# Optimization experiments

Measured on AMD Instinct MI355X. Metric: run time of the kernel, lower is better.

The kernel has to match this reference:

```python
import jax, jax.numpy as jnp
import numpy as np

B, L, C, H, W = 2, 48, 8, 48, 48


def setup_inputs() -> dict:
    key = jax.random.key(0)
    k1, k2 = jax.random.split(key)
    flows = jax.random.normal(k1, (B, L, 2, H, W), dtype=jnp.float32) * 0.05
    images = jax.random.normal(k2, (B, L, C, H, W), dtype=jnp.float32)
    return {"flows": flows, "images": images}


def _base_grid(Hh, Ww, dtype):
    step_y, step_x = 2.0 / Hh, 2.0 / Ww
    gy = jnp.linspace(-1.0 + 0.5 * step_y, 1.0 - 0.5 * step_y, Hh, dtype=dtype)
    gx = jnp.linspace(-1.0 + 0.5 * step_x, 1.0 - 0.5 * step_x, Ww, dtype=dtype)
    GX, GY = jnp.meshgrid(gx, gy, indexing="xy")  # each (H, W)
    return jnp.stack([GX, GY], axis=-1)  # (H, W, 2), channel 0 = x


def _sample_bilinear(img, ix, iy):
    # img: (C, H, W); ix, iy: (H, W) pixel coords (align_corners=False),
    # padding_mode='zeros'. 4-tap bilinear with zero outside [0, size-1].
    Hh, Ww = img.shape[1], img.shape[2]
    x0 = jnp.floor(ix)
    y0 = jnp.floor(iy)
    wx1 = ix - x0
    wy1 = iy - y0

    def tap(xf, yf, w):
        valid = (xf >= 0) & (xf <= Ww - 1) & (yf >= 0) & (yf <= Hh - 1)
        xc = jnp.clip(xf.astype(jnp.int32), 0, Ww - 1)
        yc = jnp.clip(yf.astype(jnp.int32), 0, Hh - 1)
        return img[:, yc, xc] * (w * valid)[None]

    return (tap(x0, y0, (1 - wx1) * (1 - wy1))
            + tap(x0 + 1, y0, wx1 * (1 - wy1))
            + tap(x0, y0 + 1, (1 - wx1) * wy1)
            + tap(x0 + 1, y0 + 1, wx1 * wy1))


def reference(flows, images):
    Bb, Ll, Cc, Hh, Ww = images.shape
    dtype = flows.dtype
    cum = jnp.cumsum(flows.astype(jnp.float32), axis=1).astype(dtype)  # (B,L,2,H,W)
    k_idx, t_idx = jnp.triu_indices(Ll)  # P pairs, k <= t

    base = _base_grid(Hh, Ww, dtype)  # (H,W,2)
    rel = cum[:, t_idx] - cum[:, k_idx]              # (B,P,2,H,W)
    grid = base + jnp.moveaxis(rel, 2, -1)           # (B,P,H,W,2)
    gx = jnp.remainder(grid[..., 0] + 1.0, 2.0) - 1.0  # wrap x only
    gy = grid[..., 1]
    # align_corners=False unnormalize: ((g+1)*size - 1) / 2
    ix = ((gx + 1.0) * Ww - 1.0) * 0.5
    iy = ((gy + 1.0) * Hh - 1.0) * 0.5

    src = images[:, k_idx]                           # (B,P,C,H,W)
    warped = jax.vmap(jax.vmap(_sample_bilinear))(src, ix, iy)  # (B,P,C,H,W)
    # scatter-accumulate each warped pair into its target frame t
    out = jax.vmap(lambda w: jax.ops.segment_sum(w, t_idx, num_segments=Ll))(warped)
    return out  # (B,L,C,H,W)
```

## Files before the change

kernel.cpp:

```cpp
#include <hip/hip_runtime.h>
#include <hip/hip_fp16.h>

constexpr int B = 2, L = 48, C = 8, H = 48, W = 48;
constexpr int HW = H * W;

constexpr int TPB    = 256;
constexpr int CHUNKS = HW / TPB;
constexpr int NOCT   = 6;

constexpr int OUT_ELEMS = B * L * C * HW;

constexpr int NCUM        = B * 2 * HW;
constexpr int CUM_BLOCKS  = NCUM / 256;
constexpr int NCONV       = B * L * HW;
constexpr int CONV_BLOCKS = (NCONV + 255) / 256;

__global__ void prep_kernel(const float* __restrict__ flows,
                            const float* __restrict__ images,
                            float* __restrict__ cum2,
                            __half* __restrict__ imgH) {
    if (blockIdx.x < CUM_BLOCKS) {
        int tid  = blockIdx.x * 256 + threadIdx.x;
        int pix  = tid % HW;
        int comp = (tid / HW) & 1;
        int b    = tid / (2 * HW);
        const float* src = flows + (size_t)b * L * 2 * HW + (size_t)comp * HW + pix;
        float*       dst = cum2  + ((size_t)b * L * HW + pix) * 2 + comp;
        float acc = 0.0f;
#pragma unroll
        for (int l = 0; l < L; ++l) {
            acc += src[(size_t)l * 2 * HW];
            dst[(size_t)l * HW * 2] = acc;
        }
    } else {
        int tid = (blockIdx.x - CUM_BLOCKS) * 256 + threadIdx.x;
        if (tid >= NCONV) return;
        int pix = tid % HW;
        int bl  = tid / HW;
        const float* src = images + (size_t)bl * C * HW + pix;
        __half h[C];
#pragma unroll
        for (int c = 0; c < C; ++c) h[c] = __float2half(src[(size_t)c * HW]);
        float4* dst = reinterpret_cast<float4*>(imgH + ((size_t)bl * HW + pix) * C);
        *dst = *reinterpret_cast<float4*>(h);
    }
}

struct SampleGeom {
    float w00, w10, w01, w11;
    int x0, y0;
};

__device__ __forceinline__ SampleGeom sample_geom(float base_gx_p1, float base_gy,
                                                  float relx, float rely) {
    float v = base_gx_p1 + relx;
    v = (v >= 2.0f) ? v - 2.0f : v;
    v = (v >= 2.0f) ? v - 2.0f : v;
    v = (v >= 2.0f) ? v - 2.0f : v;
    v = (v <  0.0f) ? v + 2.0f : v;
    v = (v <  0.0f) ? v + 2.0f : v;
    v = (v <  0.0f) ? v + 2.0f : v;

    float ix = (v * (float)W - 1.0f) * 0.5f;
    float gy = base_gy + rely;
    float iy = ((gy + 1.0f) * (float)H - 1.0f) * 0.5f;

    float x0f = floorf(ix), y0f = floorf(iy);
    float wx1 = ix - x0f,   wy1 = iy - y0f;
    float wx0 = 1.0f - wx1, wy0 = 1.0f - wy1;

    float vx0 = (x0f >= 0.0f  && x0f <= (float)(W - 1)) ? 1.0f : 0.0f;
    float vx1 = (x0f >= -1.0f && x0f <= (float)(W - 2)) ? 1.0f : 0.0f;
    float vy0 = (y0f >= 0.0f  && y0f <= (float)(H - 1)) ? 1.0f : 0.0f;
    float vy1 = (y0f >= -1.0f && y0f <= (float)(H - 2)) ? 1.0f : 0.0f;

    SampleGeom g;
    g.w00 = wx0 * wy0 * vx0 * vy0;
    g.w10 = wx1 * wy0 * vx1 * vy0;
    g.w01 = wx0 * wy1 * vx0 * vy1;
    g.w11 = wx1 * wy1 * vx1 * vy1;
    g.x0  = (int)x0f;
    g.y0  = (int)y0f;
    return g;
}

#if defined(__has_builtin)
#if __has_builtin(__builtin_amdgcn_global_load_lds)
#define HAVE_GLD_LDS 1
#endif
#endif

__device__ __forceinline__ void stage_frame(const __half* __restrict__ gsrc,
                                            __half* lds_base, int tid) {
#ifdef HAVE_GLD_LDS
#pragma unroll
    for (int i = 0; i < 9; ++i) {
        const int r = i * 256 + tid;
        __builtin_amdgcn_global_load_lds(
            (const __attribute__((address_space(1))) void*)(gsrc + (size_t)r * C),
            (__attribute__((address_space(3))) void*)(lds_base + (size_t)r * C),
            16, 0, 0);
    }
#else
#pragma unroll
    for (int i = 0; i < 9; ++i) {
        const int r = i * 256 + tid;
        float4 v = *reinterpret_cast<const float4*>(gsrc + (size_t)r * C);
        *reinterpret_cast<float4*>(lds_base + (size_t)r * C) = v;
    }
#endif
}

__device__ __forceinline__ void gather_mix(const __half* fb, const SampleGeom& g,
                                           float acc[C]) {
    int x0 = min(max(g.x0,     0), W - 1);
    int x1 = min(max(g.x0 + 1, 0), W - 1);
    int y0 = min(max(g.y0,     0), H - 1);
    int y1 = min(max(g.y0 + 1, 0), H - 1);
    float4 r00 = *reinterpret_cast<const float4*>(fb + (y0 * W + x0) * C);
    float4 r10 = *reinterpret_cast<const float4*>(fb + (y0 * W + x1) * C);
    float4 r01 = *reinterpret_cast<const float4*>(fb + (y1 * W + x0) * C);
    float4 r11 = *reinterpret_cast<const float4*>(fb + (y1 * W + x1) * C);
    auto mix = [&](const float4& raw, float wgt) {
        const __half2* hc = reinterpret_cast<const __half2*>(&raw);
#pragma unroll
        for (int c = 0; c < 4; ++c) {
            float2 f = __half22float2(hc[c]);
            acc[2 * c]     += wgt * f.x;
            acc[2 * c + 1] += wgt * f.y;
        }
    };
    mix(r00, g.w00); mix(r10, g.w10); mix(r01, g.w01); mix(r11, g.w11);
}

template <int P>
__global__ __launch_bounds__(256) void scan_oct_kernel(const float* __restrict__ cum2,
                                                       const __half* __restrict__ imgH,
                                                       float* __restrict__ out,
                                                       float* __restrict__ part) {
    const int tid  = threadIdx.x;
    const int pix0 = blockIdx.x * TPB;
    const int pix  = pix0 + tid;
    const int g    = blockIdx.y;
    const int par  = blockIdx.z % P;
    const int b    = blockIdx.z / P;

    int tj[8];
#pragma unroll
    for (int j = 0; j < 4; ++j) {
        tj[2 * j]     = 12 * j + g;
        tj[2 * j + 1] = 12 * j + 11 - g;
    }
    const int kmax = 47 - g;

    const int w = pix % W;
    const int h = pix / W;
    const float base_gx_p1 = (2 * w + 1) * (1.0f / W);
    const float base_gy    = (2 * h + 1) * (1.0f / H) - 1.0f;

    const float* cb = cum2 + ((size_t)b * L * HW + pix) * 2;
    float ctx[8], cty[8];
#pragma unroll
    for (int j = 0; j < 8; ++j) {
        float2 c = *reinterpret_cast<const float2*>(cb + (size_t)tj[j] * HW * 2);
        ctx[j] = c.x; cty[j] = c.y;
    }

    float acc[8][C];
#pragma unroll
    for (int j = 0; j < 8; ++j)
#pragma unroll
        for (int c = 0; c < C; ++c) acc[j][c] = 0.0f;

    __shared__ __align__(16) unsigned char smem[2 * HW * C * 2];
    __half* fr0 = reinterpret_cast<__half*>(smem);
    __half* fr1 = reinterpret_cast<__half*>(smem + HW * C * 2);

    const __half* gb = imgH + (size_t)b * L * HW * C;

    stage_frame(gb + (size_t)par * HW * C, fr0, tid);
    float2 ck = *reinterpret_cast<const float2*>(cb + (size_t)par * HW * 2);
    __syncthreads();

    int cur = 0;
    for (int k = par; k <= kmax; k += P) {
        __half* nb = cur ? fr0 : fr1;
        const __half* fb = cur ? fr1 : fr0;
        if (k + P <= kmax)
            stage_frame(gb + (size_t)(k + P) * HW * C, nb, tid);
        float2 ckn = ck;
        if (k + P <= kmax)
            ckn = *reinterpret_cast<const float2*>(cb + (size_t)(k + P) * HW * 2);

#pragma unroll
        for (int j = 0; j < 8; ++j) {
            if (tj[j] >= k) {
                SampleGeom gm = sample_geom(base_gx_p1, base_gy,
                                            ctx[j] - ck.x, cty[j] - ck.y);
                gather_mix(fb, gm, acc[j]);
            }
        }

        ck = ckn;
        __syncthreads();
        cur ^= 1;
    }

    float* accT = reinterpret_cast<float*>(smem);
#pragma unroll
    for (int j = 0; j < 8; ++j)
#pragma unroll
        for (int c = 0; c < C; ++c)
            accT[(j * 8 + c) * TPB + tid] = acc[j][c];
    __syncthreads();

    float* dst = (par == 0) ? out : (part + (size_t)(par - 1) * OUT_ELEMS);
    const int lane = tid & 63;
    const int wv   = tid >> 6;
#pragma unroll
    for (int r = 0; r < 16; ++r) {
        int pl = wv + 4 * r;
        int j  = pl >> 3, c = pl & 7;
        float4 v = *reinterpret_cast<float4*>(&accT[pl * TPB + lane * 4]);
        *reinterpret_cast<float4*>(dst + ((size_t)(b * L + tj[j]) * C + c) * HW
                                   + pix0 + lane * 4) = v;
    }
}

template <int P>
__global__ void reduce_kernel(float* __restrict__ out, const float* __restrict__ part) {
    int i = blockIdx.x * blockDim.x + threadIdx.x;
    constexpr int N4 = OUT_ELEMS / 4;
    if (i < N4) {
        float4 a = reinterpret_cast<float4*>(out)[i];
#pragma unroll
        for (int p = 0; p < P - 1; ++p) {
            float4 q = reinterpret_cast<const float4*>(part + (size_t)p * OUT_ELEMS)[i];
            a.x += q.x; a.y += q.y; a.z += q.z; a.w += q.w;
        }
        reinterpret_cast<float4*>(out)[i] = a;
    }
}

extern "C" void kernel_launch(void* const* d_in, const int* in_sizes, int n_in,
                              void* d_out, int out_size, void* d_ws, size_t ws_size,
                              hipStream_t stream) {
    const float* flows  = (const float*)d_in[0];
    const float* images = (const float*)d_in[1];
    float* out = (float*)d_out;

    const size_t cum_elems  = (size_t)B * L * 2 * HW;
    const size_t imgH_elems = (size_t)B * L * HW * C;

    float*  cum2 = (float*)d_ws;
    __half* imgH = (__half*)(cum2 + cum_elems);
    float*  part = (float*)(imgH + imgH_elems);

    const size_t base_bytes = cum_elems * 4 + imgH_elems * 2;
    const size_t out_bytes  = (size_t)OUT_ELEMS * 4;

    prep_kernel<<<CUM_BLOCKS + CONV_BLOCKS, 256, 0, stream>>>(flows, images, cum2, imgH);

    constexpr int N4 = OUT_ELEMS / 4;
    const int rblocks = (N4 + 255) / 256;

    if (ws_size >= base_bytes + 3 * out_bytes) {
        dim3 grid(CHUNKS, NOCT, 2 * 4);
        scan_oct_kernel<4><<<grid, 256, 0, stream>>>(cum2, imgH, out, part);
        reduce_kernel<4><<<rblocks, 256, 0, stream>>>(out, part);
    } else if (ws_size >= base_bytes + 2 * out_bytes) {
        dim3 grid(CHUNKS, NOCT, 2 * 3);
        scan_oct_kernel<3><<<grid, 256, 0, stream>>>(cum2, imgH, out, part);
        reduce_kernel<3><<<rblocks, 256, 0, stream>>>(out, part);
    } else {
        dim3 grid(CHUNKS, NOCT, 2 * 2);
        scan_oct_kernel<2><<<grid, 256, 0, stream>>>(cum2, imgH, out, part);
        reduce_kernel<2><<<rblocks, 256, 0, stream>>>(out, part);
    }
}
```

Measured before the change: 51.84 us.

## Generalize scan over target groups, store partial sums in half, use 8-way k split

```diff
diff --git a/kernel.cpp b/kernel.cpp
--- a/kernel.cpp
+++ b/kernel.cpp
@@ -6,7 +6,6 @@
 
 constexpr int TPB    = 256;
 constexpr int CHUNKS = HW / TPB;
-constexpr int NOCT   = 6;
 
 constexpr int OUT_ELEMS = B * L * C * HW;
 
@@ -133,11 +132,12 @@
     mix(r00, g.w00); mix(r10, g.w10); mix(r01, g.w01); mix(r11, g.w11);
 }
 
-template <int P>
-__global__ __launch_bounds__(256) void scan_oct_kernel(const float* __restrict__ cum2,
-                                                       const __half* __restrict__ imgH,
-                                                       float* __restrict__ out,
-                                                       float* __restrict__ part) {
+template <int TT, int P>
+__global__ __launch_bounds__(256) void scan_kernel(const float* __restrict__ cum2,
+                                                   const __half* __restrict__ imgH,
+                                                   float* __restrict__ out,
+                                                   __half* __restrict__ part) {
+    constexpr int S = 96 / TT;
     const int tid  = threadIdx.x;
     const int pix0 = blockIdx.x * TPB;
     const int pix  = pix0 + tid;
@@ -145,11 +145,11 @@
     const int par  = blockIdx.z % P;
     const int b    = blockIdx.z / P;
 
-    int tj[8];
-#pragma unroll
-    for (int j = 0; j < 4; ++j) {
-        tj[2 * j]     = 12 * j + g;
-        tj[2 * j + 1] = 12 * j + 11 - g;
+    int tj[TT];
+#pragma unroll
+    for (int m = 0; m < TT / 2; ++m) {
+        tj[2 * m]     = S * m + g;
+        tj[2 * m + 1] = S * m + S - 1 - g;
     }
     const int kmax = 47 - g;
 
@@ -159,16 +159,16 @@
     const float base_gy    = (2 * h + 1) * (1.0f / H) - 1.0f;
 
     const float* cb = cum2 + ((size_t)b * L * HW + pix) * 2;
-    float ctx[8], cty[8];
-#pragma unroll
-    for (int j = 0; j < 8; ++j) {
+    float ctx[TT], cty[TT];
+#pragma unroll
+    for (int j = 0; j < TT; ++j) {
         float2 c = *reinterpret_cast<const float2*>(cb + (size_t)tj[j] * HW * 2);
         ctx[j] = c.x; cty[j] = c.y;
     }
 
-    float acc[8][C];
-#pragma unroll
-    for (int j = 0; j < 8; ++j)
+    float acc[TT][C];
+#pragma unroll
+    for (int j = 0; j < TT; ++j)
 #pragma unroll
         for (int c = 0; c < C; ++c) acc[j][c] = 0.0f;
 
@@ -193,7 +193,7 @@
             ckn = *reinterpret_cast<const float2*>(cb + (size_t)(k + P) * HW * 2);
 
 #pragma unroll
-        for (int j = 0; j < 8; ++j) {
+        for (int j = 0; j < TT; ++j) {
             if (tj[j] >= k) {
                 SampleGeom gm = sample_geom(base_gx_p1, base_gy,
                                             ctx[j] - ck.x, cty[j] - ck.y);
@@ -206,37 +206,58 @@
         cur ^= 1;
     }
 
+    constexpr int NPLANES = TT * C;
+    constexpr int NROUNDS = NPLANES / 64;
     float* accT = reinterpret_cast<float*>(smem);
-#pragma unroll
-    for (int j = 0; j < 8; ++j)
-#pragma unroll
-        for (int c = 0; c < C; ++c)
-            accT[(j * 8 + c) * TPB + tid] = acc[j][c];
-    __syncthreads();
-
-    float* dst = (par == 0) ? out : (part + (size_t)(par - 1) * OUT_ELEMS);
     const int lane = tid & 63;
     const int wv   = tid >> 6;
-#pragma unroll
-    for (int r = 0; r < 16; ++r) {
-        int pl = wv + 4 * r;
-        int j  = pl >> 3, c = pl & 7;
-        float4 v = *reinterpret_cast<float4*>(&accT[pl * TPB + lane * 4]);
-        *reinterpret_cast<float4*>(dst + ((size_t)(b * L + tj[j]) * C + c) * HW
-                                   + pix0 + lane * 4) = v;
-    }
-}
-
-template <int P>
-__global__ void reduce_kernel(float* __restrict__ out, const float* __restrict__ part) {
+
+#pragma unroll
+    for (int rd = 0; rd < NROUNDS; ++rd) {
+        __syncthreads();
+#pragma unroll
+        for (int j = 0; j < TT; ++j)
+#pragma unroll
+            for (int c = 0; c < C; ++c) {
+                constexpr int dummy = 0; (void)dummy;
+                int pl = j * C + c;
+                if ((pl >> 6) == rd)
+                    accT[(pl & 63) * TPB + tid] = acc[j][c];
+            }
+        __syncthreads();
+
+#pragma unroll
+        for (int rr = 0; rr < 16; ++rr) {
+            int pl_g = rd * 64 + wv + 4 * rr;
+            int j  = pl_g >> 3, c = pl_g & 7;
+            float4 v = *reinterpret_cast<float4*>(&accT[(pl_g - rd * 64) * TPB + lane * 4]);
+            size_t off = ((size_t)(b * L + tj[j]) * C + c) * HW + pix0 + lane * 4;
+            if (par == 0) {
+                *reinterpret_cast<float4*>(out + off) = v;
+            } else {
+                __half hbuf[4];
+                hbuf[0] = __float2half(v.x); hbuf[1] = __float2half(v.y);
+                hbuf[2] = __float2half(v.z); hbuf[3] = __float2half(v.w);
+                *reinterpret_cast<float2*>(part + (size_t)(par - 1) * OUT_ELEMS + off) =
+                    *reinterpret_cast<float2*>(hbuf);
+            }
+        }
+    }
+}
+
+template <int NPART>
+__global__ void reduce_kernel(float* __restrict__ out, const __half* __restrict__ part) {
     int i = blockIdx.x * blockDim.x + threadIdx.x;
     constexpr int N4 = OUT_ELEMS / 4;
     if (i < N4) {
         float4 a = reinterpret_cast<float4*>(out)[i];
 #pragma unroll
-        for (int p = 0; p < P - 1; ++p) {
-            float4 q = reinterpret_cast<const float4*>(part + (size_t)p * OUT_ELEMS)[i];
-            a.x += q.x; a.y += q.y; a.z += q.z; a.w += q.w;
+        for (int p = 0; p < NPART; ++p) {
+            const __half2* hp = reinterpret_cast<const __half2*>(
+                part + (size_t)p * OUT_ELEMS + 4 * (size_t)i);
+            float2 f01 = __half22float2(hp[0]);
+            float2 f23 = __half22float2(hp[1]);
+            a.x += f01.x; a.y += f01.y; a.z += f23.x; a.w += f23.y;
         }
         reinterpret_cast<float4*>(out)[i] = a;
     }
@@ -254,27 +275,23 @@
 
     float*  cum2 = (float*)d_ws;
     __half* imgH = (__half*)(cum2 + cum_elems);
-    float*  part = (float*)(imgH + imgH_elems);
+    __half* part = imgH + imgH_elems;
 
     const size_t base_bytes = cum_elems * 4 + imgH_elems * 2;
-    const size_t out_bytes  = (size_t)OUT_ELEMS * 4;
+    const size_t part_bytes = (size_t)OUT_ELEMS * 2;
 
     prep_kernel<<<CUM_BLOCKS + CONV_BLOCKS, 256, 0, stream>>>(flows, images, cum2, imgH);
 
     constexpr int N4 = OUT_ELEMS / 4;
     const int rblocks = (N4 + 255) / 256;
 
-    if (ws_size >= base_bytes + 3 * out_bytes) {
-        dim3 grid(CHUNKS, NOCT, 2 * 4);
-        scan_oct_kernel<4><<<grid, 256, 0, stream>>>(cum2, imgH, out, part);
-        reduce_kernel<4><<<rblocks, 256, 0, stream>>>(out, part);
-    } else if (ws_size >= base_bytes + 2 * out_bytes) {
-        dim3 grid(CHUNKS, NOCT, 2 * 3);
-        scan_oct_kernel<3><<<grid, 256, 0, stream>>>(cum2, imgH, out, part);
+    if (ws_size >= base_bytes + 7 * part_bytes) {
+        dim3 grid(CHUNKS, 3, 2 * 8);
+        scan_kernel<16, 8><<<grid, 256, 0, stream>>>(cum2, imgH, out, part);
+        reduce_kernel<7><<<rblocks, 256, 0, stream>>>(out, part);
+    } else {
+        dim3 grid(CHUNKS, 6, 2 * 4);
+        scan_kernel<8, 4><<<grid, 256, 0, stream>>>(cum2, imgH, out, part);
         reduce_kernel<3><<<rblocks, 256, 0, stream>>>(out, part);
-    } else {
-        dim3 grid(CHUNKS, NOCT, 2 * 2);
-        scan_oct_kernel<2><<<grid, 256, 0, stream>>>(cum2, imgH, out, part);
-        reduce_kernel<2><<<rblocks, 256, 0, stream>>>(out, part);
-    }
-}
+    }
+}
```

Measured after the change: 54.20 us. 4.6% more time.
